# Optimization experiments

Measured on AMD Instinct MI355X. Metric: run time of the kernel, lower is better.

The kernel has to match this reference:

```python
import jax, jax.numpy as jnp
import numpy as np

QUERY_SHAPE = (128, 24)
MEM_FLANGE = (8, 8)
N_HEADS = 8
D_MODEL = 32


def _conv2d(x, w, b=None):
    # x: [B,H,W,Cin], w: [kh,kw,Cin,Cout], SAME padding, stride 1
    y = jax.lax.conv_general_dilated(x, w, window_strides=(1, 1), padding='SAME',
                                     dimension_numbers=('NHWC', 'HWIO', 'NHWC'))
    return y if b is None else y + b


def _local_attention_2d(q, k, v, query_shape, memory_flange):
    # q,k,v: [B, n_heads, H, W, d_head]; q is pre-scaled.
    B, n, H, W, d = q.shape
    qh, qw = query_shape
    fh, fw = memory_flange
    pad_h = (-H) % qh
    pad_w = (-W) % qw
    pad5 = ((0, 0), (0, 0), (0, pad_h), (0, pad_w), (0, 0))
    q = jnp.pad(q, pad5)
    k = jnp.pad(k, pad5)
    v = jnp.pad(v, pad5)
    Hq, Wq = H + pad_h, W + pad_w
    flange = ((0, 0), (0, 0), (fh, fh), (fw, fw), (0, 0))
    k = jnp.pad(k, flange)
    v = jnp.pad(v, flange)
    nH, nW = Hq // qh, Wq // qw
    mh, mw = qh + 2 * fh, qw + 2 * fw
    # Query blocks: [B, n, nH*nW, qh*qw, d]
    qb = q.reshape(B, n, nH, qh, nW, qw, d).transpose(0, 1, 2, 4, 3, 5, 6)
    qb = qb.reshape(B, n, nH * nW, qh * qw, d)
    # Overlapping memory blocks gathered from flange-padded k/v.
    rows = jnp.arange(nH)[:, None] * qh + jnp.arange(mh)[None, :]  # [nH, mh]
    cols = jnp.arange(nW)[:, None] * qw + jnp.arange(mw)[None, :]  # [nW, mw]
    kb = k[:, :, rows[:, None, :, None], cols[None, :, None, :], :]  # [B,n,nH,nW,mh,mw,d]
    vb = v[:, :, rows[:, None, :, None], cols[None, :, None, :], :]
    kb = kb.reshape(B, n, nH * nW, mh * mw, d)
    vb = vb.reshape(B, n, nH * nW, mh * mw, d)
    # t2t embedding_to_padding: mask positions whose key embedding is all-zero (the padding).
    bias = jnp.where(jnp.sum(jnp.abs(kb), axis=-1) == 0.0, -1e9, 0.0)[:, :, :, None, :]
    logits = jnp.einsum('bngqd,bngkd->bngqk', qb, kb) + bias
    attn = jax.nn.softmax(logits, axis=-1)
    ob = jnp.einsum('bngqk,bngkd->bngqd', attn, vb)
    out = ob.reshape(B, n, nH, nW, qh, qw, d).transpose(0, 1, 2, 4, 3, 5, 6)
    out = out.reshape(B, n, Hq, Wq, d)
    return out[:, :, :H, :W, :]


def _forward(x, wq, bq, wk, bk, wv, bv, wo):
    B, H, W, _ = x.shape
    dh = D_MODEL // N_HEADS

    def split_heads(t):  # [B,H,W,d_model] -> [B,n,H,W,dh]
        return t.reshape(B, H, W, N_HEADS, dh).transpose(0, 3, 1, 2, 4)

    q = split_heads(_conv2d(x, wq, bq)) * dh ** -0.5
    k = split_heads(_conv2d(x, wk, bk))
    v = split_heads(_conv2d(x, wv, bv))
    o = _local_attention_2d(q, k, v, QUERY_SHAPE, MEM_FLANGE)
    o = o.transpose(0, 2, 3, 1, 4).reshape(B, H, W, D_MODEL)  # combine heads
    return _conv2d(o, wo)  # no bias


def setup_inputs() -> dict:
    key = jax.random.key(0)
    ks = jax.random.split(key, 8)
    B, H, W, Cin, Cout = 1, 128, 48, 64, 64
    x = jax.random.normal(ks[0], (B, H, W, Cin), dtype=jnp.float32)

    def w(k, shape):
        fan_in = shape[0] * shape[1] * shape[2]
        return jax.random.normal(k, shape, dtype=jnp.float32) * (fan_in ** -0.5)

    return {
        'x': x,
        'wq': w(ks[1], (3, 3, Cin, D_MODEL)),
        'bq': jax.random.normal(ks[2], (D_MODEL,), dtype=jnp.float32) * 0.02,
        'wk': w(ks[3], (3, 3, Cin, D_MODEL)),
        'bk': jax.random.normal(ks[4], (D_MODEL,), dtype=jnp.float32) * 0.02,
        'wv': w(ks[5], (3, 3, Cin, D_MODEL)),
        'bv': jax.random.normal(ks[6], (D_MODEL,), dtype=jnp.float32) * 0.02,
        'wo': w(ks[7], (3, 3, D_MODEL, Cout)),
    }


def reference(x, wq, bq, wk, bk, wv, bv, wo):
    return _forward(x, wq, bq, wk, bk, wv, bv, wo)
```

## Files before the change

kernel.cpp:

```cpp
#include <hip/hip_runtime.h>

#define H_IMG 128
#define W_IMG 48
#define CIN   64
#define DM    32
#define NH    8
#define NPIX  6144
#define WPAD  50
#define HPAD  130

#define Q_SCALE 0.7213475204444817f

typedef _Float16 half4 __attribute__((ext_vector_type(4)));
typedef __fp16   fp16x2 __attribute__((ext_vector_type(2)));
typedef float    f32x4 __attribute__((ext_vector_type(4)));

__device__ __forceinline__ float fexp2(float x) { return __builtin_amdgcn_exp2f(x); }

__device__ __forceinline__ half4 exp_pack(f32x4 s) {
    fp16x2 lo = __builtin_amdgcn_cvt_pkrtz(fexp2(s[0]), fexp2(s[1]));
    fp16x2 hi = __builtin_amdgcn_cvt_pkrtz(fexp2(s[2]), fexp2(s[3]));
    half4 p;
    p[0] = (_Float16)lo[0]; p[1] = (_Float16)lo[1];
    p[2] = (_Float16)hi[0]; p[3] = (_Float16)hi[1];
    return p;
}

__global__ __launch_bounds__(256) void setup_kernel(
    const float* __restrict__ x,
    const float* __restrict__ wq, const float* __restrict__ wk,
    const float* __restrict__ wv, const float* __restrict__ wo,
    _Float16* __restrict__ xpad, _Float16* __restrict__ vT,
    _Float16* __restrict__ attpad,
    _Float16* __restrict__ whT, _Float16* __restrict__ whoT)
{
    const int u = blockIdx.x * 256 + threadIdx.x;

    if (u < 104000) {
        const int pp = u >> 4, j = u & 15;
        const int py = pp / WPAD, px = pp % WPAD;
        half4* dst = reinterpret_cast<half4*>(xpad + (size_t)pp * CIN) + j;
        if (py >= 1 && py <= H_IMG && px >= 1 && px <= W_IMG) {
            const float4 v = *reinterpret_cast<const float4*>(
                x + ((size_t)(py - 1) * W_IMG + (px - 1)) * CIN + j * 4);
            half4 hv = { (_Float16)v.x, (_Float16)v.y, (_Float16)v.z, (_Float16)v.w };
            *dst = hv;
        } else {
            const half4 z = {};
            *dst = z;
        }
    } else if (u < 156000) {
        const int t = u - 104000;
        const half4 z = {};
        reinterpret_cast<half4*>(attpad)[t] = z;
    } else if (u < 168288) {
        const int t = u - 156000;
        const int h = t / 1536, i = t % 1536;
        half4 ones = { (_Float16)1.0f, (_Float16)1.0f, (_Float16)1.0f, (_Float16)1.0f };
        reinterpret_cast<half4*>(vT + (size_t)(h * 5 + 4) * NPIX)[i] = ones;
    } else if (u < 223584) {
        const int t = u - 168288;
        const int m = t / 18432, rem = t % 18432;
        const int c = rem / 576, kidx = rem % 576;
        const int tap = kidx / 64, ci = kidx % 64;
        const float* w = (m == 0) ? wq : (m == 1) ? wk : wv;
        const float s = (m == 0) ? Q_SCALE : 1.0f;
        whT[t] = (_Float16)(w[(size_t)tap * CIN * DM + (size_t)ci * DM + c] * s);
    } else if (u < 242016) {
        const int t = u - 223584;
        const int c = t / 288, kidx = t % 288;
        const int tap = kidx / 32, ci = kidx % 32;
        whoT[t] = (_Float16)wo[(size_t)tap * DM * 64 + (size_t)ci * 64 + c];
    }
}

__global__ __launch_bounds__(192) void qkv_mfma_kernel(
    const _Float16* __restrict__ xpad,
    const _Float16* __restrict__ whT,
    const float* __restrict__ bq, const float* __restrict__ bk,
    const float* __restrict__ bv,
    half4* __restrict__ qhi, half4* __restrict__ qlo,
    half4* __restrict__ khi, half4* __restrict__ klo,
    _Float16* __restrict__ vT)
{
    __shared__ f32x4 redq[2][64];
    __shared__ _Float16 lt[2][16][20];

    const int pt  = blockIdx.x % 384;
    const int ntm = blockIdx.x / 384;
    const int nt  = ntm % 2;
    const int m   = ntm / 2;
    const int wav = __builtin_amdgcn_readfirstlane(threadIdx.x >> 6);
    const int lane = threadIdx.x & 63;
    const int r    = lane & 15;
    const int g16  = lane >> 4;

    const int p  = pt * 16 + r;
    const int y  = p / W_IMG, x0 = p % W_IMG;
    const _Float16* xb = xpad + ((size_t)y * WPAD + x0) * CIN + 4 * g16;

    const int ch = nt * 16 + r;
    const _Float16* wb = whT + ((size_t)(m * 32 + ch)) * 576 + 4 * g16;

    f32x4 acc[4] = {{0.f,0.f,0.f,0.f},{0.f,0.f,0.f,0.f},
                    {0.f,0.f,0.f,0.f},{0.f,0.f,0.f,0.f}};

    const int dy = wav;
    #pragma unroll
    for (int dx = 0; dx < 3; ++dx) {
        const int toff = (dy * WPAD + dx) * CIN;
        const int k0   = (dy * 3 + dx) * 64;
        #pragma unroll
        for (int cb = 0; cb < 4; ++cb) {
            const half4 xa = *reinterpret_cast<const half4*>(xb + toff + cb * 16);
            const half4 wf = *reinterpret_cast<const half4*>(wb + k0 + cb * 16);
            acc[cb] = __builtin_amdgcn_mfma_f32_16x16x16f16(xa, wf, acc[cb], 0, 0, 0);
        }
    }

    f32x4 o = (acc[0] + acc[1]) + (acc[2] + acc[3]);

    if (wav > 0) redq[wav - 1][lane] = o;
    __syncthreads();
    if (wav != 0) return;

    o += redq[0][lane] + redq[1][lane];

    const float* b = (m == 0) ? bq : (m == 1) ? bk : bv;
    const float bias = b[ch] * ((m == 0) ? Q_SCALE : 1.0f);
    #pragma unroll
    for (int j = 0; j < 4; ++j) o[j] += bias;

    if (m == 2) {
        const int plane = (ch >> 2) * 5 + (ch & 3);
        const int pix0 = pt * 16 + 4 * g16;
        half4 hv = { (_Float16)o[0], (_Float16)o[1], (_Float16)o[2], (_Float16)o[3] };
        *reinterpret_cast<half4*>(vT + (size_t)plane * NPIX + pix0) = hv;
    } else {
        #pragma unroll
        for (int j = 0; j < 4; ++j) {
            const float val = o[j];
            const _Float16 hi = (_Float16)val;
            const _Float16 lo = (_Float16)(val - (float)hi);
            lt[0][4 * g16 + j][r] = hi;
            lt[1][4 * g16 + j][r] = lo;
        }
        const int p4 = lane & 15;
        const int hh = lane >> 4;
        const half4 hv = *reinterpret_cast<const half4*>(&lt[0][p4][hh * 4]);
        const half4 lv = *reinterpret_cast<const half4*>(&lt[1][p4][hh * 4]);
        const int h = nt * 4 + hh;
        const size_t idx = (size_t)h * NPIX + pt * 16 + p4;
        ((half4*)((m == 0) ? qhi : khi))[idx] = hv;
        ((half4*)((m == 0) ? qlo : klo))[idx] = lv;
    }
}

__global__ __launch_bounds__(1024, 8) void attn_mfma_kernel(
    const half4* __restrict__ qhi, const half4* __restrict__ qlo,
    const half4* __restrict__ khi, const half4* __restrict__ klo,
    const _Float16* __restrict__ vT,
    _Float16* __restrict__ attpad)
{
    __shared__ f32x4 red[16][2][64];

    const int hg  = blockIdx.x / 48;
    const int qq  = blockIdx.x % 48;
    const int h   = hg >> 1, g = hg & 1;
    const int wav = __builtin_amdgcn_readfirstlane(threadIdx.x >> 6);
    const int seg = wav & 7;
    const int u   = wav >> 3;
    const int qt0 = qq * 4 + u * 2;
    const int lane = threadIdx.x & 63;
    const int c    = lane & 15;
    const int g16  = lane >> 4;
    const int c0   = g * 16;

    half4 qfA = {}, qfB = {};
    {
        const half4* qsrc = (g16 == 1) ? qlo : qhi;
        const int qa  = qt0 * 16 + c;
        const int qay = qa / 24;
        const int qb  = qa + 16;
        const int qby = qb / 24;
        if (g16 < 3) {
            qfA = qsrc[h * NPIX + qay * W_IMG + g * 24 + (qa - qay * 24)];
            qfB = qsrc[h * NPIX + qby * W_IMG + g * 24 + (qb - qby * 24)];
        }
    }

    const half4* kb = ((g16 == 2) ? klo : khi) + h * NPIX + c;
    const int vplane = (c < 4) ? c : 4;
    const _Float16* vb = vT + (h * 5 + vplane) * NPIX + 4 * g16;

    const f32x4 zc = {0.f, 0.f, 0.f, 0.f};
    f32x4 oA0 = zc, oA1 = zc, oB0 = zc, oB1 = zc;

    int koff = (seg * 16) * W_IMG + c0;
    half4 k0 = kb[koff];
    half4 k1 = kb[koff + 16];
    half4 v0 = *reinterpret_cast<const half4*>(vb + koff);
    half4 v1 = *reinterpret_cast<const half4*>(vb + koff + 16);

    #pragma unroll 4
    for (int r = 0; r < 16; ++r) {
        const int koff2 = koff + W_IMG;
        const half4 nk0 = kb[koff2];
        const half4 nk1 = kb[koff2 + 16];
        const half4 nv0 = *reinterpret_cast<const half4*>(vb + koff2);
        const half4 nv1 = *reinterpret_cast<const half4*>(vb + koff2 + 16);

        const f32x4 sA0 = __builtin_amdgcn_mfma_f32_16x16x16f16(k0, qfA, zc, 0, 0, 0);
        const f32x4 sA1 = __builtin_amdgcn_mfma_f32_16x16x16f16(k1, qfA, zc, 0, 0, 0);
        const f32x4 sB0 = __builtin_amdgcn_mfma_f32_16x16x16f16(k0, qfB, zc, 0, 0, 0);
        const f32x4 sB1 = __builtin_amdgcn_mfma_f32_16x16x16f16(k1, qfB, zc, 0, 0, 0);

        const half4 pA0 = exp_pack(sA0);
        const half4 pA1 = exp_pack(sA1);
        const half4 pB0 = exp_pack(sB0);
        const half4 pB1 = exp_pack(sB1);

        oA0 = __builtin_amdgcn_mfma_f32_16x16x16f16(pA0, v0, oA0, 0, 0, 0);
        oA1 = __builtin_amdgcn_mfma_f32_16x16x16f16(pA1, v1, oA1, 0, 0, 0);
        oB0 = __builtin_amdgcn_mfma_f32_16x16x16f16(pB0, v0, oB0, 0, 0, 0);
        oB1 = __builtin_amdgcn_mfma_f32_16x16x16f16(pB1, v1, oB1, 0, 0, 0);

        koff = koff2;
        k0 = nk0; k1 = nk1; v0 = nv0; v1 = nv1;
    }

    red[wav][0][lane] = oA0 + oA1;
    red[wav][1][lane] = oB0 + oB1;
    __syncthreads();

    if (wav < 4) {
        const int u2  = wav >> 1;
        const int t01 = wav & 1;
        f32x4 o = red[u2 * 8 + 0][t01][lane];
        #pragma unroll
        for (int s = 1; s < 8; ++s)
            o += red[u2 * 8 + s][t01][lane];

        const int baddr = (g16 * 16 + 4) << 2;
        f32x4 on;
        #pragma unroll
        for (int r = 0; r < 4; ++r) {
            const float ss = __int_as_float(
                __builtin_amdgcn_ds_bpermute(baddr, __float_as_int(o[r])));
            on[r] = o[r] * __builtin_amdgcn_rcpf(ss);
        }

        if (c < 4) {
            const int qt = qq * 4 + u2 * 2 + t01;
            #pragma unroll
            for (int r = 0; r < 4; ++r) {
                const int q  = qt * 16 + 4 * g16 + r;
                const int qy = q / 24;
                const int qx = g * 24 + (q - qy * 24);
                attpad[((size_t)(qy + 1) * WPAD + qx + 1) * DM + h * 4 + c] =
                    (_Float16)on[r];
            }
        }
    }
}

__global__ __launch_bounds__(192) void out_mfma_kernel(
    const _Float16* __restrict__ attpad,
    const _Float16* __restrict__ whoT,
    float* __restrict__ out)
{
    __shared__ f32x4 redo[2][64];

    const int pt  = blockIdx.x % 384;
    const int nt  = blockIdx.x / 384;
    const int wav = __builtin_amdgcn_readfirstlane(threadIdx.x >> 6);
    const int lane = threadIdx.x & 63;
    const int r    = lane & 15;
    const int g16  = lane >> 4;

    const int p  = pt * 16 + r;
    const int y  = p / W_IMG, x0 = p % W_IMG;
    const _Float16* ab = attpad + ((size_t)y * WPAD + x0) * DM + 4 * g16;

    const int ch = nt * 16 + r;
    const _Float16* wb = whoT + (size_t)ch * 288 + 4 * g16;

    f32x4 a0 = {0.f, 0.f, 0.f, 0.f}, a1 = {0.f, 0.f, 0.f, 0.f};

    const int dy = wav;
    #pragma unroll
    for (int dx = 0; dx < 3; ++dx) {
        const int toff = (dy * WPAD + dx) * DM;
        const int k0   = (dy * 3 + dx) * 32;
        const half4 xa0 = *reinterpret_cast<const half4*>(ab + toff);
        const half4 wf0 = *reinterpret_cast<const half4*>(wb + k0);
        a0 = __builtin_amdgcn_mfma_f32_16x16x16f16(xa0, wf0, a0, 0, 0, 0);
        const half4 xa1 = *reinterpret_cast<const half4*>(ab + toff + 16);
        const half4 wf1 = *reinterpret_cast<const half4*>(wb + k0 + 16);
        a1 = __builtin_amdgcn_mfma_f32_16x16x16f16(xa1, wf1, a1, 0, 0, 0);
    }

    f32x4 o = a0 + a1;
    if (wav > 0) redo[wav - 1][lane] = o;
    __syncthreads();
    if (wav != 0) return;

    o += redo[0][lane] + redo[1][lane];

    const int pix0 = pt * 16 + 4 * g16;
    #pragma unroll
    for (int j = 0; j < 4; ++j)
        out[(size_t)(pix0 + j) * 64 + nt * 16 + r] = o[j];
}

extern "C" void kernel_launch(void* const* d_in, const int* in_sizes, int n_in,
                              void* d_out, int out_size, void* d_ws, size_t ws_size,
                              hipStream_t stream)
{
    const float* x  = (const float*)d_in[0];
    const float* wq = (const float*)d_in[1];
    const float* bq = (const float*)d_in[2];
    const float* wk = (const float*)d_in[3];
    const float* bk = (const float*)d_in[4];
    const float* wv = (const float*)d_in[5];
    const float* bv = (const float*)d_in[6];
    const float* wo = (const float*)d_in[7];
    float* out = (float*)d_out;

    char* base = (char*)d_ws;
    half4*    qhi    = (half4*)(base + 0);
    half4*    qlo    = (half4*)(base + 393216);
    half4*    khi    = (half4*)(base + 786432);
    half4*    klo    = (half4*)(base + 1179648);
    _Float16* vT     = (_Float16*)(base + 1572864);
    _Float16* xpad   = (_Float16*)(base + 2064384);
    _Float16* attpad = (_Float16*)(base + 2896384);
    _Float16* whT    = (_Float16*)(base + 3312384);
    _Float16* whoT   = (_Float16*)(base + 3422976);

    hipLaunchKernelGGL(setup_kernel, dim3(946), dim3(256), 0, stream,
                       x, wq, wk, wv, wo, xpad, vT, attpad, whT, whoT);

    hipLaunchKernelGGL(qkv_mfma_kernel, dim3(2304), dim3(192), 0, stream,
                       xpad, whT, bq, bk, bv, qhi, qlo, khi, klo, vT);

    hipLaunchKernelGGL(attn_mfma_kernel, dim3(16 * 48), dim3(1024), 0, stream,
                       qhi, qlo, khi, klo, vT, attpad);

    hipLaunchKernelGGL(out_mfma_kernel, dim3(4 * 384), dim3(192), 0, stream,
                       attpad, whoT, out);
}
```

Baseline: 68.97 us.

## Fuse four stages into one persistent cooperative kernel with grid syncs

Result: slower. 249.0 us (+261.0%).

```diff
diff --git a/kernel.cpp b/kernel.cpp
--- a/kernel.cpp
+++ b/kernel.cpp
@@ -1,10 +1,12 @@
 #include <hip/hip_runtime.h>
+#include <hip/hip_cooperative_groups.h>
+
+namespace cg = cooperative_groups;
 
 #define H_IMG 128
 #define W_IMG 48
 #define CIN   64
 #define DM    32
-#define NH    8
 #define NPIX  6144
 #define WPAD  50
 #define HPAD  130
@@ -26,291 +28,273 @@
     return p;
 }
 
-__global__ __launch_bounds__(256) void setup_kernel(
+__global__ __launch_bounds__(512, 8) void fused_kernel(
     const float* __restrict__ x,
-    const float* __restrict__ wq, const float* __restrict__ wk,
-    const float* __restrict__ wv, const float* __restrict__ wo,
+    const float* __restrict__ wq, const float* __restrict__ bq,
+    const float* __restrict__ wk, const float* __restrict__ bk,
+    const float* __restrict__ wv, const float* __restrict__ bv,
+    const float* __restrict__ wo,
     _Float16* __restrict__ xpad, _Float16* __restrict__ vT,
     _Float16* __restrict__ attpad,
-    _Float16* __restrict__ whT, _Float16* __restrict__ whoT)
-{
-    const int u = blockIdx.x * 256 + threadIdx.x;
-
-    if (u < 104000) {
-        const int pp = u >> 4, j = u & 15;
-        const int py = pp / WPAD, px = pp % WPAD;
-        half4* dst = reinterpret_cast<half4*>(xpad + (size_t)pp * CIN) + j;
-        if (py >= 1 && py <= H_IMG && px >= 1 && px <= W_IMG) {
-            const float4 v = *reinterpret_cast<const float4*>(
-                x + ((size_t)(py - 1) * W_IMG + (px - 1)) * CIN + j * 4);
-            half4 hv = { (_Float16)v.x, (_Float16)v.y, (_Float16)v.z, (_Float16)v.w };
-            *dst = hv;
-        } else {
-            const half4 z = {};
-            *dst = z;
-        }
-    } else if (u < 156000) {
-        const int t = u - 104000;
-        const half4 z = {};
-        reinterpret_cast<half4*>(attpad)[t] = z;
-    } else if (u < 168288) {
-        const int t = u - 156000;
-        const int h = t / 1536, i = t % 1536;
-        half4 ones = { (_Float16)1.0f, (_Float16)1.0f, (_Float16)1.0f, (_Float16)1.0f };
-        reinterpret_cast<half4*>(vT + (size_t)(h * 5 + 4) * NPIX)[i] = ones;
-    } else if (u < 223584) {
-        const int t = u - 168288;
-        const int m = t / 18432, rem = t % 18432;
-        const int c = rem / 576, kidx = rem % 576;
-        const int tap = kidx / 64, ci = kidx % 64;
-        const float* w = (m == 0) ? wq : (m == 1) ? wk : wv;
-        const float s = (m == 0) ? Q_SCALE : 1.0f;
-        whT[t] = (_Float16)(w[(size_t)tap * CIN * DM + (size_t)ci * DM + c] * s);
-    } else if (u < 242016) {
-        const int t = u - 223584;
-        const int c = t / 288, kidx = t % 288;
-        const int tap = kidx / 32, ci = kidx % 32;
-        whoT[t] = (_Float16)wo[(size_t)tap * DM * 64 + (size_t)ci * 64 + c];
-    }
-}
-
-__global__ __launch_bounds__(192) void qkv_mfma_kernel(
-    const _Float16* __restrict__ xpad,
-    const _Float16* __restrict__ whT,
-    const float* __restrict__ bq, const float* __restrict__ bk,
-    const float* __restrict__ bv,
+    _Float16* __restrict__ whT, _Float16* __restrict__ whoT,
     half4* __restrict__ qhi, half4* __restrict__ qlo,
     half4* __restrict__ khi, half4* __restrict__ klo,
-    _Float16* __restrict__ vT)
+    float* __restrict__ out, int phase)
 {
-    __shared__ f32x4 redq[2][64];
-    __shared__ _Float16 lt[2][16][20];
-
-    const int pt  = blockIdx.x % 384;
-    const int ntm = blockIdx.x / 384;
-    const int nt  = ntm % 2;
-    const int m   = ntm / 2;
-    const int wav = __builtin_amdgcn_readfirstlane(threadIdx.x >> 6);
-    const int lane = threadIdx.x & 63;
+    __shared__ __align__(16) char ldsbuf[16384];
+    const int tid  = threadIdx.x;
+    const int bid  = blockIdx.x;
+    const int nb   = gridDim.x;
+    const int wav  = __builtin_amdgcn_readfirstlane(tid >> 6);
+    const int lane = tid & 63;
     const int r    = lane & 15;
     const int g16  = lane >> 4;
 
-    const int p  = pt * 16 + r;
-    const int y  = p / W_IMG, x0 = p % W_IMG;
-    const _Float16* xb = xpad + ((size_t)y * WPAD + x0) * CIN + 4 * g16;
-
-    const int ch = nt * 16 + r;
-    const _Float16* wb = whT + ((size_t)(m * 32 + ch)) * 576 + 4 * g16;
-
-    f32x4 acc[4] = {{0.f,0.f,0.f,0.f},{0.f,0.f,0.f,0.f},
-                    {0.f,0.f,0.f,0.f},{0.f,0.f,0.f,0.f}};
-
-    const int dy = wav;
-    #pragma unroll
-    for (int dx = 0; dx < 3; ++dx) {
-        const int toff = (dy * WPAD + dx) * CIN;
-        const int k0   = (dy * 3 + dx) * 64;
-        #pragma unroll
-        for (int cb = 0; cb < 4; ++cb) {
-            const half4 xa = *reinterpret_cast<const half4*>(xb + toff + cb * 16);
-            const half4 wf = *reinterpret_cast<const half4*>(wb + k0 + cb * 16);
-            acc[cb] = __builtin_amdgcn_mfma_f32_16x16x16f16(xa, wf, acc[cb], 0, 0, 0);
+    if (phase == -1 || phase == 0) {
+        for (int u = bid * 512 + tid; u < 242016; u += nb * 512) {
+            if (u < 104000) {
+                const int pp = u >> 4, j = u & 15;
+                const int py = pp / WPAD, px = pp % WPAD;
+                half4* dst = reinterpret_cast<half4*>(xpad + (size_t)pp * CIN) + j;
+                if (py >= 1 && py <= H_IMG && px >= 1 && px <= W_IMG) {
+                    const float4 v = *reinterpret_cast<const float4*>(
+                        x + ((size_t)(py - 1) * W_IMG + (px - 1)) * CIN + j * 4);
+                    half4 hv = { (_Float16)v.x, (_Float16)v.y,
+                                 (_Float16)v.z, (_Float16)v.w };
+                    *dst = hv;
+                } else {
+                    const half4 z = {};
+                    *dst = z;
+                }
+            } else if (u < 156000) {
+                const half4 z = {};
+                reinterpret_cast<half4*>(attpad)[u - 104000] = z;
+            } else if (u < 168288) {
+                const int t = u - 156000;
+                const int h = t / 1536, i = t % 1536;
+                half4 ones = { (_Float16)1.0f, (_Float16)1.0f,
+                               (_Float16)1.0f, (_Float16)1.0f };
+                reinterpret_cast<half4*>(vT + (size_t)(h * 5 + 4) * NPIX)[i] = ones;
+            } else if (u < 223584) {
+                const int t = u - 168288;
+                const int m = t / 18432, rem = t % 18432;
+                const int c = rem / 576, kidx = rem % 576;
+                const int tap = kidx / 64, ci = kidx % 64;
+                const float* w = (m == 0) ? wq : (m == 1) ? wk : wv;
+                const float s = (m == 0) ? Q_SCALE : 1.0f;
+                whT[t] = (_Float16)(w[(size_t)tap * CIN * DM + (size_t)ci * DM + c] * s);
+            } else {
+                const int t = u - 223584;
+                const int c = t / 288, kidx = t % 288;
+                const int tap = kidx / 32, ci = kidx % 32;
+                whoT[t] = (_Float16)wo[(size_t)tap * DM * 64 + (size_t)ci * 64 + c];
+            }
         }
     }
-
-    f32x4 o = (acc[0] + acc[1]) + (acc[2] + acc[3]);
-
-    if (wav > 0) redq[wav - 1][lane] = o;
-    __syncthreads();
-    if (wav != 0) return;
-
-    o += redq[0][lane] + redq[1][lane];
-
-    const float* b = (m == 0) ? bq : (m == 1) ? bk : bv;
-    const float bias = b[ch] * ((m == 0) ? Q_SCALE : 1.0f);
-    #pragma unroll
-    for (int j = 0; j < 4; ++j) o[j] += bias;
-
-    if (m == 2) {
-        const int plane = (ch >> 2) * 5 + (ch & 3);
-        const int pix0 = pt * 16 + 4 * g16;
-        half4 hv = { (_Float16)o[0], (_Float16)o[1], (_Float16)o[2], (_Float16)o[3] };
-        *reinterpret_cast<half4*>(vT + (size_t)plane * NPIX + pix0) = hv;
-    } else {
-        #pragma unroll
-        for (int j = 0; j < 4; ++j) {
-            const float val = o[j];
-            const _Float16 hi = (_Float16)val;
-            const _Float16 lo = (_Float16)(val - (float)hi);
-            lt[0][4 * g16 + j][r] = hi;
-            lt[1][4 * g16 + j][r] = lo;
+    if (phase == -1) cg::this_grid().sync();
+
+    if (phase == -1 || phase == 1) {
+        f32x4* partial = reinterpret_cast<f32x4*>(ldsbuf);
+        _Float16* ltb  = reinterpret_cast<_Float16*>(ldsbuf + 4096);
+        const int tm = wav >> 1, hf = wav & 1;
+        for (int tile = bid * 4 + tm; tile < 2304; tile += nb * 4) {
+            const int pt  = tile % 384;
+            const int ntm = tile / 384;
+            const int nt  = ntm % 2, m = ntm / 2;
+            const int p   = pt * 16 + r;
+            const int y   = p / W_IMG, x0 = p % W_IMG;
+            const _Float16* xb = xpad + ((size_t)y * WPAD + x0) * CIN + 4 * g16;
+            const int ch = nt * 16 + r;
+            const _Float16* wb = whT + ((size_t)(m * 32 + ch)) * 576 + 4 * g16;
+
+            f32x4 acc[4] = {{0,0,0,0},{0,0,0,0},{0,0,0,0},{0,0,0,0}};
+            #pragma unroll
+            for (int ii = 0; ii < 18; ++ii) {
+                const int i   = hf * 18 + ii;
+                const int tap = i >> 2, cb = i & 3;
+                const int dy  = tap / 3, dx = tap % 3;
+                const half4 xa = *reinterpret_cast<const half4*>(
+                    xb + (dy * WPAD + dx) * CIN + cb * 16);
+                const half4 wf = *reinterpret_cast<const half4*>(
+                    wb + tap * 64 + cb * 16);
+                acc[ii & 3] = __builtin_amdgcn_mfma_f32_16x16x16f16(xa, wf, acc[ii & 3], 0, 0, 0);
+            }
+            f32x4 o = (acc[0] + acc[1]) + (acc[2] + acc[3]);
+
+            if (hf == 1) partial[tm * 64 + lane] = o;
+            __syncthreads();
+            if (hf == 0) {
+                o += partial[tm * 64 + lane];
+                const float* b = (m == 0) ? bq : (m == 1) ? bk : bv;
+                const float bias = b[ch] * ((m == 0) ? Q_SCALE : 1.0f);
+                #pragma unroll
+                for (int j = 0; j < 4; ++j) o[j] += bias;
+
+                if (m == 2) {
+                    const int plane = (ch >> 2) * 5 + (ch & 3);
+                    const int pix0 = pt * 16 + 4 * g16;
+                    half4 hv = { (_Float16)o[0], (_Float16)o[1],
+                                 (_Float16)o[2], (_Float16)o[3] };
+                    *reinterpret_cast<half4*>(vT + (size_t)plane * NPIX + pix0) = hv;
+                } else {
+                    _Float16* lt = ltb + tm * 640;
+                    #pragma unroll
+                    for (int j = 0; j < 4; ++j) {
+                        const float val = o[j];
+                        const _Float16 hi = (_Float16)val;
+                        const _Float16 lo = (_Float16)(val - (float)hi);
+                        lt[(4 * g16 + j) * 20 + r]       = hi;
+                        lt[320 + (4 * g16 + j) * 20 + r] = lo;
+                    }
+                    const int p4 = lane & 15;
+                    const int hh = lane >> 4;
+                    const half4 hv = *reinterpret_cast<const half4*>(lt + p4 * 20 + hh * 4);
+                    const half4 lv = *reinterpret_cast<const half4*>(lt + 320 + p4 * 20 + hh * 4);
+                    const int h = nt * 4 + hh;
+                    const size_t idx = (size_t)h * NPIX + pt * 16 + p4;
+                    ((half4*)((m == 0) ? qhi : khi))[idx] = hv;
+                    ((half4*)((m == 0) ? qlo : klo))[idx] = lv;
+                }
+            }
+            __syncthreads();
         }
-        const int p4 = lane & 15;
-        const int hh = lane >> 4;
-        const half4 hv = *reinterpret_cast<const half4*>(&lt[0][p4][hh * 4]);
-        const half4 lv = *reinterpret_cast<const half4*>(&lt[1][p4][hh * 4]);
-        const int h = nt * 4 + hh;
-        const size_t idx = (size_t)h * NPIX + pt * 16 + p4;
-        ((half4*)((m == 0) ? qhi : khi))[idx] = hv;
-        ((half4*)((m == 0) ? qlo : klo))[idx] = lv;
-    }
-}
-
-__global__ __launch_bounds__(1024, 8) void attn_mfma_kernel(
-    const half4* __restrict__ qhi, const half4* __restrict__ qlo,
-    const half4* __restrict__ khi, const half4* __restrict__ klo,
-    const _Float16* __restrict__ vT,
-    _Float16* __restrict__ attpad)
-{
-    __shared__ f32x4 red[16][2][64];
-
-    const int hg  = blockIdx.x / 48;
-    const int qq  = blockIdx.x % 48;
-    const int h   = hg >> 1, g = hg & 1;
-    const int wav = __builtin_amdgcn_readfirstlane(threadIdx.x >> 6);
-    const int seg = wav & 7;
-    const int u   = wav >> 3;
-    const int qt0 = qq * 4 + u * 2;
-    const int lane = threadIdx.x & 63;
-    const int c    = lane & 15;
-    const int g16  = lane >> 4;
-    const int c0   = g * 16;
-
-    half4 qfA = {}, qfB = {};
-    {
-        const half4* qsrc = (g16 == 1) ? qlo : qhi;
-        const int qa  = qt0 * 16 + c;
-        const int qay = qa / 24;
-        const int qb  = qa + 16;
-        const int qby = qb / 24;
-        if (g16 < 3) {
-            qfA = qsrc[h * NPIX + qay * W_IMG + g * 24 + (qa - qay * 24)];
-            qfB = qsrc[h * NPIX + qby * W_IMG + g * 24 + (qb - qby * 24)];
+    }
+    if (phase == -1) cg::this_grid().sync();
+
+    if (phase == -1 || phase == 2) {
+        f32x4* red = reinterpret_cast<f32x4*>(ldsbuf);
+        for (int ub = bid; ub < 768; ub += nb) {
+            const int hg = ub / 48;
+            const int qq = ub % 48;
+            const int h = hg >> 1, g = hg & 1;
+            const int seg = wav >> 1;
+            const int u   = wav & 1;
+            const int qt0 = qq * 4 + u * 2;
+            const int c   = r;
+            const int c0  = g * 16;
+
+            half4 qfA = {}, qfB = {};
+            {
+                const half4* qsrc = (g16 == 1) ? qlo : qhi;
+                const int qa  = qt0 * 16 + c;
+                const int qay = qa / 24;
+                const int qb  = qa + 16;
+                const int qby = qb / 24;
+                if (g16 < 3) {
+                    qfA = qsrc[h * NPIX + qay * W_IMG + g * 24 + (qa - qay * 24)];
+                    qfB = qsrc[h * NPIX + qby * W_IMG + g * 24 + (qb - qby * 24)];
+                }
+            }
+
+            const half4* kb = ((g16 == 2) ? klo : khi) + h * NPIX + c;
+            const int vplane = (c < 4) ? c : 4;
+            const _Float16* vb = vT + (h * 5 + vplane) * NPIX + 4 * g16;
+
+            const f32x4 zc = {0.f, 0.f, 0.f, 0.f};
+            f32x4 oA0 = zc, oA1 = zc, oB0 = zc, oB1 = zc;
+
+            const int r0 = seg * 32;
+            #pragma unroll 4
+            for (int rr = 0; rr < 32; ++rr) {
+                const int koff = (r0 + rr) * W_IMG + c0;
+
+                const half4 k0 = kb[koff];
+                const half4 k1 = kb[koff + 16];
+                const half4 v0 = *reinterpret_cast<const half4*>(vb + koff);
+                const half4 v1 = *reinterpret_cast<const half4*>(vb + koff + 16);
+
+                const f32x4 sA0 = __builtin_amdgcn_mfma_f32_16x16x16f16(k0, qfA, zc, 0, 0, 0);
+                const f32x4 sA1 = __builtin_amdgcn_mfma_f32_16x16x16f16(k1, qfA, zc, 0, 0, 0);
+                const f32x4 sB0 = __builtin_amdgcn_mfma_f32_16x16x16f16(k0, qfB, zc, 0, 0, 0);
+                const f32x4 sB1 = __builtin_amdgcn_mfma_f32_16x16x16f16(k1, qfB, zc, 0, 0, 0);
+
+                const half4 pA0 = exp_pack(sA0);
+                const half4 pA1 = exp_pack(sA1);
+                const half4 pB0 = exp_pack(sB0);
+                const half4 pB1 = exp_pack(sB1);
+
+                oA0 = __builtin_amdgcn_mfma_f32_16x16x16f16(pA0, v0, oA0, 0, 0, 0);
+                oA1 = __builtin_amdgcn_mfma_f32_16x16x16f16(pA1, v1, oA1, 0, 0, 0);
+                oB0 = __builtin_amdgcn_mfma_f32_16x16x16f16(pB0, v0, oB0, 0, 0, 0);
+                oB1 = __builtin_amdgcn_mfma_f32_16x16x16f16(pB1, v1, oB1, 0, 0, 0);
+            }
+
+            red[(wav * 2 + 0) * 64 + lane] = oA0 + oA1;
+            red[(wav * 2 + 1) * 64 + lane] = oB0 + oB1;
+            __syncthreads();
+
+            if (wav < 4) {
+                const int t = seg;
+                f32x4 o = red[((0 + u) * 2 + t) * 64 + lane];
+                o += red[((2 + u) * 2 + t) * 64 + lane];
+                o += red[((4 + u) * 2 + t) * 64 + lane];
+                o += red[((6 + u) * 2 + t) * 64 + lane];
+
+                const int baddr = (g16 * 16 + 4) << 2;
+                f32x4 on;
+                #pragma unroll
+                for (int j = 0; j < 4; ++j) {
+                    const float ss = __int_as_float(
+                        __builtin_amdgcn_ds_bpermute(baddr, __float_as_int(o[j])));
+                    on[j] = o[j] * __builtin_amdgcn_rcpf(ss);
+                }
+
+                if (c < 4) {
+                    const int qt = qt0 + t;
+                    #pragma unroll
+                    for (int j = 0; j < 4; ++j) {
+                        const int q  = qt * 16 + 4 * g16 + j;
+                        const int qy = q / 24;
+                        const int qx = g * 24 + (q - qy * 24);
+                        attpad[((size_t)(qy + 1) * WPAD + qx + 1) * DM + h * 4 + c] =
+                            (_Float16)on[j];
+                    }
+                }
+            }
+            __syncthreads();
         }
     }
-
-    const half4* kb = ((g16 == 2) ? klo : khi) + h * NPIX + c;
-    const int vplane = (c < 4) ? c : 4;
-    const _Float16* vb = vT + (h * 5 + vplane) * NPIX + 4 * g16;
-
-    const f32x4 zc = {0.f, 0.f, 0.f, 0.f};
-    f32x4 oA0 = zc, oA1 = zc, oB0 = zc, oB1 = zc;
-
-    int koff = (seg * 16) * W_IMG + c0;
-    half4 k0 = kb[koff];
-    half4 k1 = kb[koff + 16];
-    half4 v0 = *reinterpret_cast<const half4*>(vb + koff);
-    half4 v1 = *reinterpret_cast<const half4*>(vb + koff + 16);
-
-    #pragma unroll 4
-    for (int r = 0; r < 16; ++r) {
-        const int koff2 = koff + W_IMG;
-        const half4 nk0 = kb[koff2];
-        const half4 nk1 = kb[koff2 + 16];
-        const half4 nv0 = *reinterpret_cast<const half4*>(vb + koff2);
-        const half4 nv1 = *reinterpret_cast<const half4*>(vb + koff2 + 16);
-
-        const f32x4 sA0 = __builtin_amdgcn_mfma_f32_16x16x16f16(k0, qfA, zc, 0, 0, 0);
-        const f32x4 sA1 = __builtin_amdgcn_mfma_f32_16x16x16f16(k1, qfA, zc, 0, 0, 0);
-        const f32x4 sB0 = __builtin_amdgcn_mfma_f32_16x16x16f16(k0, qfB, zc, 0, 0, 0);
-        const f32x4 sB1 = __builtin_amdgcn_mfma_f32_16x16x16f16(k1, qfB, zc, 0, 0, 0);
-
-        const half4 pA0 = exp_pack(sA0);
-        const half4 pA1 = exp_pack(sA1);
-        const half4 pB0 = exp_pack(sB0);
-        const half4 pB1 = exp_pack(sB1);
-
-        oA0 = __builtin_amdgcn_mfma_f32_16x16x16f16(pA0, v0, oA0, 0, 0, 0);
-        oA1 = __builtin_amdgcn_mfma_f32_16x16x16f16(pA1, v1, oA1, 0, 0, 0);
-        oB0 = __builtin_amdgcn_mfma_f32_16x16x16f16(pB0, v0, oB0, 0, 0, 0);
-        oB1 = __builtin_amdgcn_mfma_f32_16x16x16f16(pB1, v1, oB1, 0, 0, 0);
-
-        koff = koff2;
-        k0 = nk0; k1 = nk1; v0 = nv0; v1 = nv1;
-    }
-
-    red[wav][0][lane] = oA0 + oA1;
-    red[wav][1][lane] = oB0 + oB1;
-    __syncthreads();
-
-    if (wav < 4) {
-        const int u2  = wav >> 1;
-        const int t01 = wav & 1;
-        f32x4 o = red[u2 * 8 + 0][t01][lane];
-        #pragma unroll
-        for (int s = 1; s < 8; ++s)
-            o += red[u2 * 8 + s][t01][lane];
-
-        const int baddr = (g16 * 16 + 4) << 2;
-        f32x4 on;
-        #pragma unroll
-        for (int r = 0; r < 4; ++r) {
-            const float ss = __int_as_float(
-                __builtin_amdgcn_ds_bpermute(baddr, __float_as_int(o[r])));
-            on[r] = o[r] * __builtin_amdgcn_rcpf(ss);
+    if (phase == -1) cg::this_grid().sync();
+
+    if (phase == -1 || phase == 3) {
+        f32x4* po = reinterpret_cast<f32x4*>(ldsbuf);
+        const int tm = wav >> 1, hf = wav & 1;
+        for (int tile = bid * 4 + tm; tile < 1536; tile += nb * 4) {
+            const int pt = tile % 384;
+            const int nt = tile / 384;
+            const int p  = pt * 16 + r;
+            const int y  = p / W_IMG, x0 = p % W_IMG;
+            const _Float16* ab = attpad + ((size_t)y * WPAD + x0) * DM + 4 * g16;
+            const int ch = nt * 16 + r;
+            const _Float16* wb = whoT + (size_t)ch * 288 + 4 * g16;
+
+            f32x4 a0 = {0,0,0,0}, a1 = {0,0,0,0};
+            #pragma unroll
+            for (int ii = 0; ii < 9; ++ii) {
+                const int i   = hf * 9 + ii;
+                const int tap = i >> 1, cb = i & 1;
+                const int dy  = tap / 3, dx = tap % 3;
+                const half4 xa = *reinterpret_cast<const half4*>(
+                    ab + (dy * WPAD + dx) * DM + cb * 16);
+                const half4 wf = *reinterpret_cast<const half4*>(
+                    wb + tap * 32 + cb * 16);
+                if (ii & 1) a1 = __builtin_amdgcn_mfma_f32_16x16x16f16(xa, wf, a1, 0, 0, 0);
+                else        a0 = __builtin_amdgcn_mfma_f32_16x16x16f16(xa, wf, a0, 0, 0, 0);
+            }
+            f32x4 o = a0 + a1;
+
+            if (hf == 1) po[tm * 64 + lane] = o;
+            __syncthreads();
+            if (hf == 0) {
+                o += po[tm * 64 + lane];
+                const int pix0 = pt * 16 + 4 * g16;
+                #pragma unroll
+                for (int j = 0; j < 4; ++j)
+                    out[(size_t)(pix0 + j) * 64 + nt * 16 + r] = o[j];
+            }
+            __syncthreads();
         }
-
-        if (c < 4) {
-            const int qt = qq * 4 + u2 * 2 + t01;
-            #pragma unroll
-            for (int r = 0; r < 4; ++r) {
-                const int q  = qt * 16 + 4 * g16 + r;
-                const int qy = q / 24;
-                const int qx = g * 24 + (q - qy * 24);
-                attpad[((size_t)(qy + 1) * WPAD + qx + 1) * DM + h * 4 + c] =
-                    (_Float16)on[r];
-            }
-        }
-    }
-}
-
-__global__ __launch_bounds__(192) void out_mfma_kernel(
-    const _Float16* __restrict__ attpad,
-    const _Float16* __restrict__ whoT,
-    float* __restrict__ out)
-{
-    __shared__ f32x4 redo[2][64];
-
-    const int pt  = blockIdx.x % 384;
-    const int nt  = blockIdx.x / 384;
-    const int wav = __builtin_amdgcn_readfirstlane(threadIdx.x >> 6);
-    const int lane = threadIdx.x & 63;
-    const int r    = lane & 15;
-    const int g16  = lane >> 4;
-
-    const int p  = pt * 16 + r;
-    const int y  = p / W_IMG, x0 = p % W_IMG;
-    const _Float16* ab = attpad + ((size_t)y * WPAD + x0) * DM + 4 * g16;
-
-    const int ch = nt * 16 + r;
-    const _Float16* wb = whoT + (size_t)ch * 288 + 4 * g16;
-
-    f32x4 a0 = {0.f, 0.f, 0.f, 0.f}, a1 = {0.f, 0.f, 0.f, 0.f};
-
-    const int dy = wav;
-    #pragma unroll
-    for (int dx = 0; dx < 3; ++dx) {
-        const int toff = (dy * WPAD + dx) * DM;
-        const int k0   = (dy * 3 + dx) * 32;
-        const half4 xa0 = *reinterpret_cast<const half4*>(ab + toff);
-        const half4 wf0 = *reinterpret_cast<const half4*>(wb + k0);
-        a0 = __builtin_amdgcn_mfma_f32_16x16x16f16(xa0, wf0, a0, 0, 0, 0);
-        const half4 xa1 = *reinterpret_cast<const half4*>(ab + toff + 16);
-        const half4 wf1 = *reinterpret_cast<const half4*>(wb + k0 + 16);
-        a1 = __builtin_amdgcn_mfma_f32_16x16x16f16(xa1, wf1, a1, 0, 0, 0);
-    }
-
-    f32x4 o = a0 + a1;
-    if (wav > 0) redo[wav - 1][lane] = o;
-    __syncthreads();
-    if (wav != 0) return;
-
-    o += redo[0][lane] + redo[1][lane];
-
-    const int pix0 = pt * 16 + 4 * g16;
-    #pragma unroll
-    for (int j = 0; j < 4; ++j)
-        out[(size_t)(pix0 + j) * 64 + nt * 16 + r] = o[j];
+    }
 }
 
 extern "C" void kernel_launch(void* const* d_in, const int* in_sizes, int n_in,
@@ -338,15 +322,34 @@
     _Float16* whT    = (_Float16*)(base + 3312384);
     _Float16* whoT   = (_Float16*)(base + 3422976);
 
-    hipLaunchKernelGGL(setup_kernel, dim3(946), dim3(256), 0, stream,
-                       x, wq, wk, wv, wo, xpad, vT, attpad, whT, whoT);
-
-    hipLaunchKernelGGL(qkv_mfma_kernel, dim3(2304), dim3(192), 0, stream,
-                       xpad, whT, bq, bk, bv, qhi, qlo, khi, klo, vT);
-
-    hipLaunchKernelGGL(attn_mfma_kernel, dim3(16 * 48), dim3(1024), 0, stream,
-                       qhi, qlo, khi, klo, vT, attpad);
-
-    hipLaunchKernelGGL(out_mfma_kernel, dim3(4 * 384), dim3(192), 0, stream,
-                       attpad, whoT, out);
+    int dev = 0;
+    hipGetDevice(&dev);
+    int coop = 0;
+    hipDeviceGetAttribute(&coop, hipDeviceAttributeCooperativeLaunch, dev);
+    int maxb = 0;
+    hipOccupancyMaxActiveBlocksPerMultiprocessor(&maxb, fused_kernel, 512, 0);
+
+    bool done = false;
+    int phase = -1;
+    if (coop && maxb > 0) {
+        int nblk = maxb * 256;
+        if (nblk > 1024) nblk = 1024;
+        void* args[] = {
+            (void*)&x, (void*)&wq, (void*)&bq, (void*)&wk, (void*)&bk,
+            (void*)&wv, (void*)&bv, (void*)&wo,
+            (void*)&xpad, (void*)&vT, (void*)&attpad, (void*)&whT, (void*)&whoT,
+            (void*)&qhi, (void*)&qlo, (void*)&khi, (void*)&klo,
+            (void*)&out, (void*)&phase
+        };
+        if (hipLaunchCooperativeKernel((const void*)fused_kernel, dim3(nblk),
+                                       dim3(512), args, 0, stream) == hipSuccess)
+            done = true;
+    }
+    if (!done) {
+        for (int ph = 0; ph < 4; ++ph)
+            hipLaunchKernelGGL(fused_kernel, dim3(1024), dim3(512), 0, stream,
+                               x, wq, bq, wk, bk, wv, bv, wo,
+                               xpad, vT, attpad, whT, whoT,
+                               qhi, qlo, khi, klo, out, ph);
+    }
 }
```
